# Kernel tuning notes

Hardware: AMD Instinct MI355X
Metric: run time of the kernel (lower is better)

Reference implementation:

```python
import jax, jax.numpy as jnp
import numpy as np


def _laplacian(A):
    # D^{-1/2} A D^{-1/2}; original builds diag matrices and does D@A@D,
    # which is mathematically identical to broadcast row/col scaling.
    d = jnp.sum(A, axis=-1)
    dinv = 1.0 / jnp.sqrt(d)
    return A * dinv[:, None] * dinv[None, :]


def _poly(A, theta):
    # P = I + sum_{i=1..k} theta_sig[i-1] * A^i  (theta passed through sigmoid)
    t = jax.nn.sigmoid(theta)
    N = A.shape[-1]
    P = jnp.eye(N, dtype=A.dtype)
    seg = P
    for i in range(theta.shape[0]):  # k is small (2), static loop over poly order
        seg = seg @ A
        P = P + seg * t[i]
    return P


def setup_inputs() -> dict:
    key = jax.random.key(0)
    k1, k2, k3, k4 = jax.random.split(key, 4)
    N, DIN, DOUT, K_CHEB = 4096, 64, 64, 2
    return {
        "x": jax.random.normal(k1, (N, DIN), dtype=jnp.float32),
        "A": jax.random.uniform(k2, (N, N), dtype=jnp.float32),  # positive row sums
        "theta": jax.random.normal(k3, (K_CHEB,), dtype=jnp.float32),
        "W": jax.random.normal(k4, (DOUT, DIN), dtype=jnp.float32) / np.float32(np.sqrt(DIN)),
        "b": jnp.zeros((DOUT,), dtype=jnp.float32),
        "k": 4,
    }


def reference(x, A, theta, W, b, k):
    S = _laplacian(A)
    S = _poly(S, theta)
    S = _laplacian(S)
    # double argsort over last dim = per-row descending rank of each entry
    rank = jnp.argsort(jnp.argsort(-S, axis=-1), axis=-1)
    mask = jnp.where(rank < k, jnp.float32(1.0), jnp.float32(0.0))
    S = S * mask  # keep only top-k entries per row
    x = S @ x     # [N,N] @ [N,DIN]
    return x @ W.T + b  # nn.Linear
```

## Files before the change

### kernel.cpp

```cpp
#include <hip/hip_runtime.h>
#include <hip/hip_bf16.h>
#include <float.h>
#include <math.h>

#define N 4096
#define DIN 64

typedef signed char i8_t;
typedef signed char i8x4 __attribute__((ext_vector_type(4)));
typedef int i32x4 __attribute__((ext_vector_type(4)));
typedef float f32x4 __attribute__((ext_vector_type(4)));

__device__ __forceinline__ void gload16(const void* g, void* l) {
    __builtin_amdgcn_global_load_lds((const __attribute__((address_space(1))) void*)g,
                                     (__attribute__((address_space(3))) void*)l,
                                     16, 0, 0);
}

__device__ __forceinline__ float block_reduce_sum(float s) {
    __shared__ float red[4];
    #pragma unroll
    for (int off = 32; off; off >>= 1) s += __shfl_down(s, off);
    if ((threadIdx.x & 63) == 0) red[threadIdx.x >> 6] = s;
    __syncthreads();
    return red[0] + red[1] + red[2] + red[3];
}

__device__ __forceinline__ float2 block_reduce_sum2(float a, float b) {
    __shared__ float reda[4], redb[4];
    #pragma unroll
    for (int off = 32; off; off >>= 1) { a += __shfl_down(a, off); b += __shfl_down(b, off); }
    if ((threadIdx.x & 63) == 0) { reda[threadIdx.x >> 6] = a; redb[threadIdx.x >> 6] = b; }
    __syncthreads();
    float2 r;
    r.x = reda[0] + reda[1] + reda[2] + reda[3];
    r.y = redb[0] + redb[1] + redb[2] + redb[3];
    return r;
}

__device__ __forceinline__ bool better(float v1, int j1, float v2, int j2) {
    return v1 > v2 || (v1 == v2 && j1 < j2);
}
__device__ __forceinline__ void ins4(float v, int j, float bv[4], int bj[4]) {
    if (!better(v, j, bv[3], bj[3])) return;
    bv[3] = v; bj[3] = j;
    if (better(bv[3], bj[3], bv[2], bj[2])) {
        float tv = bv[2]; int tj = bj[2]; bv[2] = bv[3]; bj[2] = bj[3]; bv[3] = tv; bj[3] = tj;
    }
    if (better(bv[2], bj[2], bv[1], bj[1])) {
        float tv = bv[1]; int tj = bj[1]; bv[1] = bv[2]; bj[1] = bj[2]; bv[2] = tv; bj[2] = tj;
    }
    if (better(bv[1], bj[1], bv[0], bj[0])) {
        float tv = bv[0]; int tj = bj[0]; bv[0] = bv[1]; bj[0] = bj[1]; bv[1] = tv; bj[1] = tj;
    }
}

__global__ __launch_bounds__(256) void k_rowsum_dinv(const float* __restrict__ A,
                                                     float* __restrict__ dinv,
                                                     int* __restrict__ dmax_i,
                                                     float* __restrict__ colsumQ) {
    int row = blockIdx.x, tid = threadIdx.x;
    const float4* a4 = (const float4*)(A + (size_t)row * N);
    float s = 0.f;
    for (int j = tid; j < N / 4; j += 256) {
        float4 v = a4[j];
        s += v.x + v.y + v.z + v.w;
    }
    float tot = block_reduce_sum(s);
    if (tid == 0) {
        float v = rsqrtf(tot);
        dinv[row] = v;
        atomicMax(dmax_i, __float_as_int(v));
        colsumQ[row] = 0.f;
    }
}

__global__ __launch_bounds__(256) void k_make_sqt(const float* __restrict__ A,
                                                  const float* __restrict__ dinv,
                                                  const int* __restrict__ dmax_i,
                                                  i8_t* __restrict__ Sq,
                                                  i8_t* __restrict__ Tq,
                                                  float* __restrict__ colsumQ) {
    __shared__ float tile[64][65];
    int tid = threadIdx.x;
    int c4 = tid & 15;
    int rg = tid >> 4;
    int i0 = blockIdx.y * 64;
    int j0 = blockIdx.x * 64;
    float dmax = __int_as_float(*dmax_i);
    float sinv = 127.0f / (dmax * dmax);
    float4 dj = *(const float4*)(dinv + j0 + 4 * c4);
    #pragma unroll
    for (int rr = 0; rr < 4; rr++) {
        int r = rg + 16 * rr;
        int row = i0 + r;
        float di = dinv[row];
        float4 av = *(const float4*)(A + (size_t)row * N + j0 + 4 * c4);
        float s0 = av.x * di * dj.x, s1 = av.y * di * dj.y;
        float s2 = av.z * di * dj.z, s3 = av.w * di * dj.w;
        i8x4 qv;
        qv[0] = (i8_t)(int)fminf(rintf(s0 * sinv), 127.f);
        qv[1] = (i8_t)(int)fminf(rintf(s1 * sinv), 127.f);
        qv[2] = (i8_t)(int)fminf(rintf(s2 * sinv), 127.f);
        qv[3] = (i8_t)(int)fminf(rintf(s3 * sinv), 127.f);
        *(i8x4*)(Sq + (size_t)row * N + j0 + 4 * c4) = qv;
        tile[r][4 * c4 + 0] = s0;
        tile[r][4 * c4 + 1] = s1;
        tile[r][4 * c4 + 2] = s2;
        tile[r][4 * c4 + 3] = s3;
    }
    __syncthreads();
    #pragma unroll
    for (int cc = 0; cc < 4; cc++) {
        int c = rg + 16 * cc;
        int gj = j0 + c;
        i8x4 qv;
        int psum = 0;
        #pragma unroll
        for (int u = 0; u < 4; u++) {
            qv[u] = (i8_t)(int)fminf(rintf(tile[4 * c4 + u][c] * sinv), 127.f);
            psum += (int)qv[u];
        }
        *(i8x4*)(Tq + (size_t)gj * N + i0 + 4 * c4) = qv;
        float fs = (float)psum;
        fs += __shfl_xor(fs, 1);
        fs += __shfl_xor(fs, 2);
        fs += __shfl_xor(fs, 4);
        fs += __shfl_xor(fs, 8);
        if (c4 == 0) atomicAdd(&colsumQ[gj], fs);
    }
}

__global__ __launch_bounds__(256) void k_dinv2row(const i8_t* __restrict__ Sq,
                                                  const float* __restrict__ colsumQ,
                                                  const int* __restrict__ dmax_i,
                                                  const float* __restrict__ theta,
                                                  float* __restrict__ dinv2) {
    int row = blockIdx.x, tid = threadIdx.x;
    int4 w = ((const int4*)(Sq + (size_t)row * N))[tid];
    float dot = 0.f, rq = 0.f;
    #pragma unroll
    for (int u = 0; u < 4; u++) {
        int wv = (u == 0) ? w.x : (u == 1) ? w.y : (u == 2) ? w.z : w.w;
        float4 cv = ((const float4*)colsumQ)[tid * 4 + u];
        float q0 = (float)(i8_t)(wv), q1 = (float)(i8_t)(wv >> 8);
        float q2 = (float)(i8_t)(wv >> 16), q3 = (float)(i8_t)(wv >> 24);
        dot += q0 * cv.x + q1 * cv.y + q2 * cv.z + q3 * cv.w;
        rq += q0 + q1 + q2 + q3;
    }
    float2 tot = block_reduce_sum2(dot, rq);
    if (tid == 0) {
        float dmax = __int_as_float(*dmax_i);
        float sqv = dmax * dmax / 127.0f;
        float t0 = 1.f / (1.f + expf(-theta[0]));
        float t1 = 1.f / (1.f + expf(-theta[1]));
        dinv2[row] = rsqrtf(t1 * sqv * sqv * tot.x + t0 * sqv * tot.y + 1.f);
    }
}

__global__ __launch_bounds__(256) void k_gemm(const i8_t* __restrict__ Sq,
                                              const i8_t* __restrict__ Tq,
                                              const int* __restrict__ dmax_i,
                                              const float* __restrict__ theta,
                                              const float* __restrict__ dinv2,
                                              float* __restrict__ candV,
                                              int* __restrict__ candJ) {
    __shared__ __align__(16) char smem[128 * 65 * 4];
    i8_t* As = (i8_t*)smem;
    i8_t* Bs = (i8_t*)(smem + 16384);
    float (*pbuf)[65] = (float (*)[65])smem;
    int tid = threadIdx.x;
    int lane = tid & 63;
    int wave = tid >> 6;
    int wr = wave >> 1, wc = wave & 1;
    int bi = blockIdx.x, bj = blockIdx.y;

    int qch = ((tid & 7) ^ ((tid >> 3) & 7)) * 16;
    int row0 = tid >> 3;
    const i8_t* Ag = Sq + (size_t)(bi * 128 + row0) * N + qch;
    const i8_t* Bg = Tq + (size_t)(bj * 128 + row0) * N + qch;
    i8_t* Al = As + tid * 16;
    i8_t* Bl = Bs + tid * 16;
    const size_t rstep = (size_t)32 * N;

    i32x4 acc[4][4];
    i32x4 z = {0, 0, 0, 0};
    #pragma unroll
    for (int i = 0; i < 4; i++)
        #pragma unroll
        for (int j = 0; j < 4; j++) acc[i][j] = z;

    int r = lane & 15, quad = lane >> 4;
    int rx = r & 7;
    int abase = (wr * 64 + r) * 128;
    int bbase = (wc * 64 + r) * 128;

    for (int k0 = 0; k0 < N; k0 += 128) {
        __syncthreads();
        gload16(Ag + k0, Al);
        gload16(Ag + k0 + rstep, Al + 4096);
        gload16(Ag + k0 + 2 * rstep, Al + 8192);
        gload16(Ag + k0 + 3 * rstep, Al + 12288);
        gload16(Bg + k0, Bl);
        gload16(Bg + k0 + rstep, Bl + 4096);
        gload16(Bg + k0 + 2 * rstep, Bl + 8192);
        gload16(Bg + k0 + 3 * rstep, Bl + 12288);
        __syncthreads();
        #pragma unroll
        for (int kk = 0; kk < 2; kk++) {
            int coff = ((kk * 4 + quad) ^ rx) * 16;
            i32x4 af[4], bfr[4];
            #pragma unroll
            for (int mi = 0; mi < 4; mi++) af[mi] = *(const i32x4*)(As + abase + mi * 2048 + coff);
            #pragma unroll
            for (int ni = 0; ni < 4; ni++) bfr[ni] = *(const i32x4*)(Bs + bbase + ni * 2048 + coff);
            #pragma unroll
            for (int mi = 0; mi < 4; mi++)
                #pragma unroll
                for (int ni = 0; ni < 4; ni++)
                    acc[mi][ni] = __builtin_amdgcn_mfma_i32_16x16x64_i8(af[mi], bfr[ni],
                                                                        acc[mi][ni], 0, 0, 0);
        }
    }
    __syncthreads();

    float dmax = __int_as_float(*dmax_i);
    float sqv = dmax * dmax / 127.0f;
    float t0 = 1.f / (1.f + expf(-theta[0]));
    float t1 = 1.f / (1.f + expf(-theta[1]));
    float t0s = t0 * sqv;
    float t1s2 = t1 * sqv * sqv;
    int col = lane & 15;

    #pragma unroll
    for (int mi = 0; mi < 4; mi++) {
        int gi0 = bi * 128 + wr * 64 + mi * 16 + quad * 4;
        #pragma unroll
        for (int ni = 0; ni < 4; ni++) {
            int gj = bj * 128 + wc * 64 + ni * 16 + col;
            float djv = dinv2[gj];
            f32x4 pf;
            #pragma unroll
            for (int rr = 0; rr < 4; rr++) {
                int gi = gi0 + rr;
                float qv = (float)Sq[(size_t)gi * N + gj];
                float p = t1s2 * (float)acc[mi][ni][rr] + t0s * qv + ((gi == gj) ? 1.f : 0.f);
                pf[rr] = p * djv;
            }
            acc[mi][ni] = __builtin_bit_cast(i32x4, pf);
        }
    }

    float bv[4] = {-FLT_MAX, -FLT_MAX, -FLT_MAX, -FLT_MAX};
    int bjx[4] = {N, N, N, N};
    int srow = tid >> 1;
    int shalf = tid & 1;

    #pragma unroll
    for (int pass = 0; pass < 2; pass++) {
        if (wc == pass) {
            #pragma unroll
            for (int mi = 0; mi < 4; mi++) {
                int prow = wr * 64 + mi * 16 + quad * 4;
                #pragma unroll
                for (int ni = 0; ni < 4; ni++) {
                    f32x4 pf = __builtin_bit_cast(f32x4, acc[mi][ni]);
                    #pragma unroll
                    for (int rr = 0; rr < 4; rr++)
                        pbuf[prow + rr][ni * 16 + col] = pf[rr];
                }
            }
        }
        __syncthreads();
        int jbase = bj * 128 + pass * 64 + shalf * 32;
        for (int i = 0; i < 32; i++)
            ins4(pbuf[srow][shalf * 32 + i], jbase + i, bv, bjx);
        __syncthreads();
    }

    float ov[4]; int oj[4];
    #pragma unroll
    for (int c = 0; c < 4; c++) { ov[c] = __shfl_xor(bv[c], 1); oj[c] = __shfl_xor(bjx[c], 1); }
    #pragma unroll
    for (int c = 0; c < 4; c++) ins4(ov[c], oj[c], bv, bjx);
    if (shalf == 0) {
        size_t base = ((size_t)(bi * 128 + srow) * 32 + bj) * 4;
        #pragma unroll
        for (int c = 0; c < 4; c++) { candV[base + c] = bv[c]; candJ[base + c] = bjx[c]; }
    }
}

__global__ __launch_bounds__(64) void k_final(const float* __restrict__ candV,
                                              const int* __restrict__ candJ,
                                              const float* __restrict__ dinv2,
                                              const float* __restrict__ x,
                                              const float* __restrict__ W,
                                              const float* __restrict__ bvec,
                                              const int* __restrict__ kin,
                                              float* __restrict__ out) {
    int row = blockIdx.x, t = threadIdx.x;
    float2 cv = *(const float2*)(candV + (size_t)row * 128 + t * 2);
    int2 cj = *(const int2*)(candJ + (size_t)row * 128 + t * 2);
    float bv[4] = {-FLT_MAX, -FLT_MAX, -FLT_MAX, -FLT_MAX};
    int bj[4] = {N, N, N, N};
    ins4(cv.x, cj.x, bv, bj);
    ins4(cv.y, cj.y, bv, bj);
    #pragma unroll
    for (int off = 1; off < 64; off <<= 1) {
        float ov[4]; int oj[4];
        #pragma unroll
        for (int c = 0; c < 4; c++) { ov[c] = __shfl_xor(bv[c], off); oj[c] = __shfl_xor(bj[c], off); }
        #pragma unroll
        for (int c = 0; c < 4; c++) ins4(ov[c], oj[c], bv, bj);
    }
    int kk = kin[0];
    if (kk > 4) kk = 4;
    if (kk < 0) kk = 0;
    float sc = dinv2[row];
    float y = 0.f;
    for (int c = 0; c < kk; c++)
        y += sc * bv[c] * x[(size_t)bj[c] * DIN + t];
    __shared__ float ys[DIN];
    ys[t] = y;
    __syncthreads();
    const float4* w4 = (const float4*)(W + (size_t)t * DIN);
    const float4* y4 = (const float4*)ys;
    float o = bvec[t];
    #pragma unroll
    for (int d = 0; d < DIN / 4; d++) {
        float4 wv = w4[d], yv = y4[d];
        o += wv.x * yv.x + wv.y * yv.y + wv.z * yv.z + wv.w * yv.w;
    }
    out[(size_t)row * DIN + t] = o;
}

extern "C" void kernel_launch(void* const* d_in, const int* in_sizes, int n_in,
                              void* d_out, int out_size, void* d_ws, size_t ws_size,
                              hipStream_t stream) {
    const float* x = (const float*)d_in[0];
    const float* A = (const float*)d_in[1];
    const float* theta = (const float*)d_in[2];
    const float* W = (const float*)d_in[3];
    const float* b = (const float*)d_in[4];
    const int* kin = (const int*)d_in[5];
    float* out = (float*)d_out;

    char* ws = (char*)d_ws;
    i8_t* Sq = (i8_t*)ws;
    i8_t* Tq = (i8_t*)(ws + (size_t)N * N);
    float* candV = (float*)(ws + (size_t)N * N * 2);
    int* candJ = (int*)(ws + (size_t)N * N * 2 + (size_t)N * 128 * 4);
    float* dinv = (float*)(ws + (size_t)N * N * 2 + (size_t)N * 128 * 8);
    float* dinv2 = dinv + N;
    float* colsumQ = dinv2 + N;
    int* dmax_i = (int*)(colsumQ + N);

    k_rowsum_dinv<<<N, 256, 0, stream>>>(A, dinv, dmax_i, colsumQ);
    k_make_sqt<<<dim3(64, 64), 256, 0, stream>>>(A, dinv, dmax_i, Sq, Tq, colsumQ);
    k_dinv2row<<<N, 256, 0, stream>>>(Sq, colsumQ, dmax_i, theta, dinv2);
    k_gemm<<<dim3(32, 32), 256, 0, stream>>>(Sq, Tq, dmax_i, theta, dinv2, candV, candJ);
    k_final<<<N, 64, 0, stream>>>(candV, candJ, dinv2, x, W, b, kin, out);
}
```

Measured before the change: 301.3 us.

## Shrink GEMM K-tile, stage Sq epilogue tile in LDS, widen quantize stores

The int8 GEMM main loop now uses a 64-wide K tile with a new XOR swizzle, which halves the LDS footprint per iteration but doubles the number of barrier pairs. The epilogue now loads the Sq block into LDS with async global-to-LDS copies instead of doing scattered byte loads from global memory per accumulator element. dinv2 values are hoisted into registers. The quantize/transpose kernel now has each thread handle 16 contiguous bytes, so it writes 16-byte vectors instead of 4-byte ones and needs fewer shuffles.

```diff
diff --git a/kernel.cpp b/kernel.cpp
--- a/kernel.cpp
+++ b/kernel.cpp
@@ -8,6 +8,7 @@
 
 typedef signed char i8_t;
 typedef signed char i8x4 __attribute__((ext_vector_type(4)));
+typedef signed char i8x16 __attribute__((ext_vector_type(16)));
 typedef int i32x4 __attribute__((ext_vector_type(4)));
 typedef float f32x4 __attribute__((ext_vector_type(4)));
 
@@ -83,51 +84,53 @@
                                                   float* __restrict__ colsumQ) {
     __shared__ float tile[64][65];
     int tid = threadIdx.x;
-    int c4 = tid & 15;
-    int rg = tid >> 4;
+    int c16 = tid & 3;
+    int rg = tid >> 2;
     int i0 = blockIdx.y * 64;
     int j0 = blockIdx.x * 64;
     float dmax = __int_as_float(*dmax_i);
     float sinv = 127.0f / (dmax * dmax);
-    float4 dj = *(const float4*)(dinv + j0 + 4 * c4);
-    #pragma unroll
-    for (int rr = 0; rr < 4; rr++) {
-        int r = rg + 16 * rr;
-        int row = i0 + r;
+
+    {
+        int row = i0 + rg;
         float di = dinv[row];
-        float4 av = *(const float4*)(A + (size_t)row * N + j0 + 4 * c4);
-        float s0 = av.x * di * dj.x, s1 = av.y * di * dj.y;
-        float s2 = av.z * di * dj.z, s3 = av.w * di * dj.w;
-        i8x4 qv;
-        qv[0] = (i8_t)(int)fminf(rintf(s0 * sinv), 127.f);
-        qv[1] = (i8_t)(int)fminf(rintf(s1 * sinv), 127.f);
-        qv[2] = (i8_t)(int)fminf(rintf(s2 * sinv), 127.f);
-        qv[3] = (i8_t)(int)fminf(rintf(s3 * sinv), 127.f);
-        *(i8x4*)(Sq + (size_t)row * N + j0 + 4 * c4) = qv;
-        tile[r][4 * c4 + 0] = s0;
-        tile[r][4 * c4 + 1] = s1;
-        tile[r][4 * c4 + 2] = s2;
-        tile[r][4 * c4 + 3] = s3;
-    }
-    __syncthreads();
-    #pragma unroll
-    for (int cc = 0; cc < 4; cc++) {
-        int c = rg + 16 * cc;
-        int gj = j0 + c;
-        i8x4 qv;
+        const float4* a4 = (const float4*)(A + (size_t)row * N + j0 + 16 * c16);
+        const float4* dj4 = (const float4*)(dinv + j0 + 16 * c16);
+        i8x16 qv;
+        #pragma unroll
+        for (int u4 = 0; u4 < 4; u4++) {
+            float4 av = a4[u4];
+            float4 dj = dj4[u4];
+            float s0 = av.x * di * dj.x, s1 = av.y * di * dj.y;
+            float s2 = av.z * di * dj.z, s3 = av.w * di * dj.w;
+            qv[4 * u4 + 0] = (i8_t)(int)fminf(rintf(s0 * sinv), 127.f);
+            qv[4 * u4 + 1] = (i8_t)(int)fminf(rintf(s1 * sinv), 127.f);
+            qv[4 * u4 + 2] = (i8_t)(int)fminf(rintf(s2 * sinv), 127.f);
+            qv[4 * u4 + 3] = (i8_t)(int)fminf(rintf(s3 * sinv), 127.f);
+            tile[rg][16 * c16 + 4 * u4 + 0] = s0;
+            tile[rg][16 * c16 + 4 * u4 + 1] = s1;
+            tile[rg][16 * c16 + 4 * u4 + 2] = s2;
+            tile[rg][16 * c16 + 4 * u4 + 3] = s3;
+        }
+        *(i8x16*)(Sq + (size_t)row * N + j0 + 16 * c16) = qv;
+    }
+    __syncthreads();
+    {
+        int c16t = tid & 3, cg = tid >> 2;
+        int gj = j0 + cg;
+        i8x16 qv;
         int psum = 0;
         #pragma unroll
-        for (int u = 0; u < 4; u++) {
-            qv[u] = (i8_t)(int)fminf(rintf(tile[4 * c4 + u][c] * sinv), 127.f);
-            psum += (int)qv[u];
+        for (int u = 0; u < 16; u++) {
+            int qq = (int)fminf(rintf(tile[16 * c16t + u][cg] * sinv), 127.f);
+            qv[u] = (i8_t)qq;
+            psum += qq;
         }
-        *(i8x4*)(Tq + (size_t)gj * N + i0 + 4 * c4) = qv;
+        *(i8x16*)(Tq + (size_t)gj * N + i0 + 16 * c16t) = qv;
         float fs = (float)psum;
         fs += __shfl_xor(fs, 1);
         fs += __shfl_xor(fs, 2);
-        fs += __shfl_xor(fs, 4);
-        fs += __shfl_xor(fs, 8);
-        if (c4 == 0) atomicAdd(&colsumQ[gj], fs);
+        if (c16t == 0) atomicAdd(&colsumQ[gj], fs);
     }
 }
 
@@ -167,7 +170,8 @@
                                               int* __restrict__ candJ) {
     __shared__ __align__(16) char smem[128 * 65 * 4];
     i8_t* As = (i8_t*)smem;
-    i8_t* Bs = (i8_t*)(smem + 16384);
+    i8_t* Bs = (i8_t*)(smem + 128 * 64);
+    i8_t* Qs = (i8_t*)smem;
     float (*pbuf)[65] = (float (*)[65])smem;
     int tid = threadIdx.x;
     int lane = tid & 63;
@@ -175,13 +179,16 @@
     int wr = wave >> 1, wc = wave & 1;
     int bi = blockIdx.x, bj = blockIdx.y;
 
-    int qch = ((tid & 7) ^ ((tid >> 3) & 7)) * 16;
-    int row0 = tid >> 3;
-    const i8_t* Ag = Sq + (size_t)(bi * 128 + row0) * N + qch;
-    const i8_t* Bg = Tq + (size_t)(bj * 128 + row0) * N + qch;
-    i8_t* Al = As + tid * 16;
-    i8_t* Bl = Bs + tid * 16;
-    const size_t rstep = (size_t)32 * N;
+    int qoff = ((tid & 3) ^ ((tid >> 3) & 3)) * 16;
+    int row0 = tid >> 2;
+    const i8_t* Ag0 = Sq + (size_t)(bi * 128 + row0) * N + qoff;
+    const i8_t* Ag1 = Sq + (size_t)(bi * 128 + 64 + row0) * N + qoff;
+    const i8_t* Bg0 = Tq + (size_t)(bj * 128 + row0) * N + qoff;
+    const i8_t* Bg1 = Tq + (size_t)(bj * 128 + 64 + row0) * N + qoff;
+    i8_t* Al0 = As + tid * 16;
+    i8_t* Al1 = As + (tid + 256) * 16;
+    i8_t* Bl0 = Bs + tid * 16;
+    i8_t* Bl1 = Bs + (tid + 256) * 16;
 
     i32x4 acc[4][4];
     i32x4 z = {0, 0, 0, 0};
@@ -190,37 +197,40 @@
         #pragma unroll
         for (int j = 0; j < 4; j++) acc[i][j] = z;
 
-    int r = lane & 15, quad = lane >> 4;
-    int rx = r & 7;
-    int abase = (wr * 64 + r) * 128;
-    int bbase = (wc * 64 + r) * 128;
-
-    for (int k0 = 0; k0 < N; k0 += 128) {
+    int r = lane & 15, q = lane >> 4;
+    int qs = q ^ ((r >> 1) & 3);
+    int aoff = (wr * 64 + r) * 64 + qs * 16;
+    int boff = (wc * 64 + r) * 64 + qs * 16;
+
+    for (int k0 = 0; k0 < N; k0 += 64) {
         __syncthreads();
-        gload16(Ag + k0, Al);
-        gload16(Ag + k0 + rstep, Al + 4096);
-        gload16(Ag + k0 + 2 * rstep, Al + 8192);
-        gload16(Ag + k0 + 3 * rstep, Al + 12288);
-        gload16(Bg + k0, Bl);
-        gload16(Bg + k0 + rstep, Bl + 4096);
-        gload16(Bg + k0 + 2 * rstep, Bl + 8192);
-        gload16(Bg + k0 + 3 * rstep, Bl + 12288);
+        gload16(Ag0 + k0, Al0);
+        gload16(Ag1 + k0, Al1);
+        gload16(Bg0 + k0, Bl0);
+        gload16(Bg1 + k0, Bl1);
         __syncthreads();
-        #pragma unroll
-        for (int kk = 0; kk < 2; kk++) {
-            int coff = ((kk * 4 + quad) ^ rx) * 16;
-            i32x4 af[4], bfr[4];
+        i32x4 af[4], bfr[4];
+        #pragma unroll
+        for (int mi = 0; mi < 4; mi++) af[mi] = *(const i32x4*)(As + aoff + mi * 16 * 64);
+        #pragma unroll
+        for (int ni = 0; ni < 4; ni++) bfr[ni] = *(const i32x4*)(Bs + boff + ni * 16 * 64);
+        #pragma unroll
+        for (int mi = 0; mi < 4; mi++)
             #pragma unroll
-            for (int mi = 0; mi < 4; mi++) af[mi] = *(const i32x4*)(As + abase + mi * 2048 + coff);
-            #pragma unroll
-            for (int ni = 0; ni < 4; ni++) bfr[ni] = *(const i32x4*)(Bs + bbase + ni * 2048 + coff);
-            #pragma unroll
-            for (int mi = 0; mi < 4; mi++)
-                #pragma unroll
-                for (int ni = 0; ni < 4; ni++)
-                    acc[mi][ni] = __builtin_amdgcn_mfma_i32_16x16x64_i8(af[mi], bfr[ni],
-                                                                        acc[mi][ni], 0, 0, 0);
-        }
+            for (int ni = 0; ni < 4; ni++)
+                acc[mi][ni] = __builtin_amdgcn_mfma_i32_16x16x64_i8(af[mi], bfr[ni],
+                                                                    acc[mi][ni], 0, 0, 0);
+    }
+    __syncthreads();
+
+    {
+        int gch = ((tid & 7) ^ ((tid >> 3) & 7)) * 16;
+        const i8_t* Qg = Sq + (size_t)(bi * 128 + (tid >> 3)) * N + bj * 128 + gch;
+        i8_t* Ql = Qs + tid * 16;
+        gload16(Qg, Ql);
+        gload16(Qg + (size_t)32 * N, Ql + 4096);
+        gload16(Qg + (size_t)64 * N, Ql + 8192);
+        gload16(Qg + (size_t)96 * N, Ql + 12288);
     }
     __syncthreads();
 
@@ -230,26 +240,35 @@
     float t1 = 1.f / (1.f + expf(-theta[1]));
     float t0s = t0 * sqv;
     float t1s2 = t1 * sqv * sqv;
-    int col = lane & 15;
+    int col = lane & 15, quad = lane >> 4;
+
+    float djv4[4];
+    #pragma unroll
+    for (int ni = 0; ni < 4; ni++)
+        djv4[ni] = dinv2[bj * 128 + wc * 64 + ni * 16 + col];
 
     #pragma unroll
     for (int mi = 0; mi < 4; mi++) {
         int gi0 = bi * 128 + wr * 64 + mi * 16 + quad * 4;
+        int rowL0 = wr * 64 + mi * 16 + quad * 4;
         #pragma unroll
         for (int ni = 0; ni < 4; ni++) {
             int gj = bj * 128 + wc * 64 + ni * 16 + col;
-            float djv = dinv2[gj];
+            int chnk = wc * 4 + ni;
             f32x4 pf;
             #pragma unroll
             for (int rr = 0; rr < 4; rr++) {
                 int gi = gi0 + rr;
-                float qv = (float)Sq[(size_t)gi * N + gj];
+                int rowL = rowL0 + rr;
+                int qaddr = rowL * 128 + ((chnk ^ (rowL & 7)) << 4) + col;
+                float qv = (float)Qs[qaddr];
                 float p = t1s2 * (float)acc[mi][ni][rr] + t0s * qv + ((gi == gj) ? 1.f : 0.f);
-                pf[rr] = p * djv;
+                pf[rr] = p * djv4[ni];
             }
             acc[mi][ni] = __builtin_bit_cast(i32x4, pf);
         }
     }
+    __syncthreads();
 
     float bv[4] = {-FLT_MAX, -FLT_MAX, -FLT_MAX, -FLT_MAX};
     int bjx[4] = {N, N, N, N};
```

Result: no change. 301.0 us (-0.1%).

## Halve GEMM K-tile to 64 and remap blocks for L2 locality

Applied to the files above, without the earlier changes.

The int8 GEMM now stages a 64-wide K slice per iteration instead of 128, which halves the LDS footprint and uses a new XOR swizzle for the smaller tile. The 2D grid becomes a 1D grid whose block index is remapped so that groups of row tiles sharing B columns run close together, aiming to improve L2 reuse. Lower LDS use could raise occupancy, but the loop now has twice as many iterations and barriers, with fewer MFMAs between each sync.

```diff
diff --git a/kernel.cpp b/kernel.cpp
--- a/kernel.cpp
+++ b/kernel.cpp
@@ -167,21 +167,26 @@
                                               int* __restrict__ candJ) {
     __shared__ __align__(16) char smem[128 * 65 * 4];
     i8_t* As = (i8_t*)smem;
-    i8_t* Bs = (i8_t*)(smem + 16384);
+    i8_t* Bs = (i8_t*)(smem + 128 * 64);
     float (*pbuf)[65] = (float (*)[65])smem;
     int tid = threadIdx.x;
     int lane = tid & 63;
     int wave = tid >> 6;
     int wr = wave >> 1, wc = wave & 1;
-    int bi = blockIdx.x, bj = blockIdx.y;
-
-    int qch = ((tid & 7) ^ ((tid >> 3) & 7)) * 16;
-    int row0 = tid >> 3;
-    const i8_t* Ag = Sq + (size_t)(bi * 128 + row0) * N + qch;
-    const i8_t* Bg = Tq + (size_t)(bj * 128 + row0) * N + qch;
-    i8_t* Al = As + tid * 16;
-    i8_t* Bl = Bs + tid * 16;
-    const size_t rstep = (size_t)32 * N;
+    int n = blockIdx.x;
+    int bi = (n & 7) * 4 + ((n >> 3) & 3);
+    int bj = n >> 5;
+
+    int qoff = ((tid & 3) ^ ((tid >> 3) & 3)) * 16;
+    int row0 = tid >> 2;
+    const i8_t* Ag0 = Sq + (size_t)(bi * 128 + row0) * N + qoff;
+    const i8_t* Ag1 = Sq + (size_t)(bi * 128 + 64 + row0) * N + qoff;
+    const i8_t* Bg0 = Tq + (size_t)(bj * 128 + row0) * N + qoff;
+    const i8_t* Bg1 = Tq + (size_t)(bj * 128 + 64 + row0) * N + qoff;
+    i8_t* Al0 = As + tid * 16;
+    i8_t* Al1 = As + (tid + 256) * 16;
+    i8_t* Bl0 = Bs + tid * 16;
+    i8_t* Bl1 = Bs + (tid + 256) * 16;
 
     i32x4 acc[4][4];
     i32x4 z = {0, 0, 0, 0};
@@ -190,37 +195,29 @@
         #pragma unroll
         for (int j = 0; j < 4; j++) acc[i][j] = z;
 
-    int r = lane & 15, quad = lane >> 4;
-    int rx = r & 7;
-    int abase = (wr * 64 + r) * 128;
-    int bbase = (wc * 64 + r) * 128;
-
-    for (int k0 = 0; k0 < N; k0 += 128) {
+    int r = lane & 15, q = lane >> 4;
+    int qs = q ^ ((r >> 1) & 3);
+    int aoff = (wr * 64 + r) * 64 + qs * 16;
+    int boff = (wc * 64 + r) * 64 + qs * 16;
+
+    for (int k0 = 0; k0 < N; k0 += 64) {
         __syncthreads();
-        gload16(Ag + k0, Al);
-        gload16(Ag + k0 + rstep, Al + 4096);
-        gload16(Ag + k0 + 2 * rstep, Al + 8192);
-        gload16(Ag + k0 + 3 * rstep, Al + 12288);
-        gload16(Bg + k0, Bl);
-        gload16(Bg + k0 + rstep, Bl + 4096);
-        gload16(Bg + k0 + 2 * rstep, Bl + 8192);
-        gload16(Bg + k0 + 3 * rstep, Bl + 12288);
+        gload16(Ag0 + k0, Al0);
+        gload16(Ag1 + k0, Al1);
+        gload16(Bg0 + k0, Bl0);
+        gload16(Bg1 + k0, Bl1);
         __syncthreads();
-        #pragma unroll
-        for (int kk = 0; kk < 2; kk++) {
-            int coff = ((kk * 4 + quad) ^ rx) * 16;
-            i32x4 af[4], bfr[4];
+        i32x4 af[4], bfr[4];
+        #pragma unroll
+        for (int mi = 0; mi < 4; mi++) af[mi] = *(const i32x4*)(As + aoff + mi * 16 * 64);
+        #pragma unroll
+        for (int ni = 0; ni < 4; ni++) bfr[ni] = *(const i32x4*)(Bs + boff + ni * 16 * 64);
+        #pragma unroll
+        for (int mi = 0; mi < 4; mi++)
             #pragma unroll
-            for (int mi = 0; mi < 4; mi++) af[mi] = *(const i32x4*)(As + abase + mi * 2048 + coff);
-            #pragma unroll
-            for (int ni = 0; ni < 4; ni++) bfr[ni] = *(const i32x4*)(Bs + bbase + ni * 2048 + coff);
-            #pragma unroll
-            for (int mi = 0; mi < 4; mi++)
-                #pragma unroll
-                for (int ni = 0; ni < 4; ni++)
-                    acc[mi][ni] = __builtin_amdgcn_mfma_i32_16x16x64_i8(af[mi], bfr[ni],
-                                                                        acc[mi][ni], 0, 0, 0);
-        }
+            for (int ni = 0; ni < 4; ni++)
+                acc[mi][ni] = __builtin_amdgcn_mfma_i32_16x16x64_i8(af[mi], bfr[ni],
+                                                                    acc[mi][ni], 0, 0, 0);
     }
     __syncthreads();
 
@@ -230,7 +227,7 @@
     float t1 = 1.f / (1.f + expf(-theta[1]));
     float t0s = t0 * sqv;
     float t1s2 = t1 * sqv * sqv;
-    int col = lane & 15;
+    int col = lane & 15, quad = lane >> 4;
 
     #pragma unroll
     for (int mi = 0; mi < 4; mi++) {
@@ -358,6 +355,6 @@
     k_rowsum_dinv<<<N, 256, 0, stream>>>(A, dinv, dmax_i, colsumQ);
     k_make_sqt<<<dim3(64, 64), 256, 0, stream>>>(A, dinv, dmax_i, Sq, Tq, colsumQ);
     k_dinv2row<<<N, 256, 0, stream>>>(Sq, colsumQ, dmax_i, theta, dinv2);
-    k_gemm<<<dim3(32, 32), 256, 0, stream>>>(Sq, Tq, dmax_i, theta, dinv2, candV, candJ);
+    k_gemm<<<1024, 256, 0, stream>>>(Sq, Tq, dmax_i, theta, dinv2, candV, candJ);
     k_final<<<N, 64, 0, stream>>>(candV, candJ, dinv2, x, W, b, kin, out);
 }
```

Result: no change. 305.0 us (+1.2%).
